# Performance work log

Measured on AMD Instinct MI355X. Metric: run time of the kernel, lower is better.

The kernel has to match this reference:

```python
import jax, jax.numpy as jnp
import numpy as np


def setup_inputs() -> dict:
    key = jax.random.key(0)
    k1, k2 = jax.random.split(key)
    x = jax.random.normal(k1, (1, 48, 56, 56), dtype=jnp.float32)
    w = jax.random.normal(k2, (24, 96, 7), dtype=jnp.float32)
    return {"x": x, "w": w, "shift": 1}


def reference(x, w, shift):
    # The torch unfold + einsum is a grouped cross-correlation along W:
    #   x viewed as (1, groups=2, Cin=24, H=56, W=56)
    #   out[l,o,k,n,m] = sum_{i,j} x[l,o,i,n, m+j-3] * w[i,k,j]   (zero-padded)
    # Same weight w is shared by both groups -> duplicate it per group.
    wt = jnp.transpose(w, (1, 0, 2))               # (96, 24, 7)  OIK per group
    kernel = jnp.concatenate([wt, wt], axis=0)     # (192, 24, 7) both groups
    kernel = kernel[:, :, None, :]                 # (O=192, I=24, KH=1, KW=7)
    y = jax.lax.conv_general_dilated(
        x, kernel,
        window_strides=(1, 1),
        padding=((0, 0), (3, 3)),                  # 'same' along W only
        dimension_numbers=("NCHW", "OIHW", "NCHW"),
        feature_group_count=2,
    )                                              # (1, 192, 56, 56)
    # torch.roll(t, shift, dims=2): roll along H
    return jnp.roll(y, shift, axis=2)
```

## Files before the change

### kernel.cpp

```cpp
#include <hip/hip_runtime.h>


#define Hh 56
#define Wd 56
#define HWsz (Hh * Wd)
#define CI 24
#define KW 7
#define OCB 4

__global__ __launch_bounds__(128) void conv7_roll_kernel(
    const float* __restrict__ x,
    const float* __restrict__ w,
    const int* __restrict__ shift_p,
    float* __restrict__ out)
{
    const int tid  = threadIdx.x;
    const int wid  = tid >> 6;
    const int lane = tid & 63;
    const int rl   = lane >> 4;
    const int c4r  = lane & 15;
    const int c4   = c4r < 13 ? c4r : 13;

    const int obase = blockIdx.x * OCB;
    const int g     = obase / 96;
    const int ocb96 = obase - g * 96;

    __shared__ __align__(16) float wl[OCB * CI * 8];
    for (int t = tid; t < OCB * CI * 8; t += 128) {
        const int oc_l = t / (CI * 8);
        const int rem  = t - oc_l * (CI * 8);
        const int ci   = rem >> 3;
        const int k    = rem & 7;
        wl[t] = (k < KW) ? w[ci * (96 * KW) + (ocb96 + oc_l) * KW + k] : 0.0f;
    }
    __syncthreads();

    const int shift = shift_p[0];
    const int h_out = blockIdx.y * 4 + rl;
    int hi = (h_out - shift) % Hh;
    if (hi < 0) hi += Hh;

    const float* xp = x + g * (CI * HWsz) + hi * Wd + c4 * 4;
    const float* lp = xp + (c4 > 0  ? -4 : 0);
    const float* rp = xp + (c4 < 13 ?  4 : 0);
    const bool lz = (c4 == 0);
    const bool rz = (c4 >= 13);

    const float* wl0 = &wl[(wid * 2    ) * (CI * 8)];
    const float* wl1 = &wl[(wid * 2 + 1) * (CI * 8)];

    float a0[4] = {0.f, 0.f, 0.f, 0.f};
    float a1[4] = {0.f, 0.f, 0.f, 0.f};

    #pragma unroll 4
    for (int ci = 0; ci < CI; ++ci) {
        float4 M = *(const float4*)(xp + ci * HWsz);
        float4 L = *(const float4*)(lp + ci * HWsz);
        float4 R = *(const float4*)(rp + ci * HWsz);
        if (lz) { L.x = 0.f; L.y = 0.f; L.z = 0.f; L.w = 0.f; }
        if (rz) { R.x = 0.f; R.y = 0.f; R.z = 0.f; R.w = 0.f; }
        float xv[12] = {L.x, L.y, L.z, L.w, M.x, M.y, M.z, M.w, R.x, R.y, R.z, R.w};

        float4 wa = *(const float4*)(wl0 + ci * 8);
        float4 wb = *(const float4*)(wl0 + ci * 8 + 4);
        float4 wc = *(const float4*)(wl1 + ci * 8);
        float4 wd = *(const float4*)(wl1 + ci * 8 + 4);
        float w0[7] = {wa.x, wa.y, wa.z, wa.w, wb.x, wb.y, wb.z};
        float w1[7] = {wc.x, wc.y, wc.z, wc.w, wd.x, wd.y, wd.z};

        #pragma unroll
        for (int k = 0; k < KW; ++k) {
            #pragma unroll
            for (int j = 0; j < 4; ++j) {
                a0[j] += xv[1 + j + k] * w0[k];
                a1[j] += xv[1 + j + k] * w1[k];
            }
        }
    }

    if (c4r < 14) {
        const int o0 = obase + wid * 2;
        float* op0 = out + o0 * HWsz + h_out * Wd + c4 * 4;
        float* op1 = op0 + HWsz;
        *(float4*)op0 = make_float4(a0[0], a0[1], a0[2], a0[3]);
        *(float4*)op1 = make_float4(a1[0], a1[1], a1[2], a1[3]);
    }
}

extern "C" void kernel_launch(void* const* d_in, const int* in_sizes, int n_in,
                              void* d_out, int out_size, void* d_ws, size_t ws_size,
                              hipStream_t stream)
{
    const float* x     = (const float*)d_in[0];
    const float* w     = (const float*)d_in[1];
    const int*   shift = (const int*)d_in[2];
    float*       out   = (float*)d_out;

    dim3 grid(48, 14);
    conv7_roll_kernel<<<grid, 128, 0, stream>>>(x, w, shift, out);
}
```

Baseline: 68.66 us.

## Share neighbor pixels via DPP lane shifts and prefetch input channels into registers

The left and right neighbor float4 global loads are replaced with DPP row_shr/row_shl lane shifts of the centre vector. Each 16-lane row covers one image row, and bound_ctrl zeroes the edge lanes to act as padding. This cuts input loads per channel from three to one. A 12-deep register ring buffer of input channels is also issued before the weight staging and barrier, so global latency overlaps the shared-memory fill. The cost is more register pressure from a fully unrolled loop holding 12 float4 prefetches.

```diff
diff --git a/kernel.cpp b/kernel.cpp
--- a/kernel.cpp
+++ b/kernel.cpp
@@ -7,6 +7,16 @@
 #define CI 24
 #define KW 7
 #define OCB 4
+#define PF 12
+
+__device__ __forceinline__ float dpp_shr1(float v) {
+    return __int_as_float(__builtin_amdgcn_update_dpp(
+        0, __float_as_int(v), 0x111, 0xF, 0xF, true));
+}
+__device__ __forceinline__ float dpp_shl1(float v) {
+    return __int_as_float(__builtin_amdgcn_update_dpp(
+        0, __float_as_int(v), 0x101, 0xF, 0xF, true));
+}
 
 __global__ __launch_bounds__(128) void conv7_roll_kernel(
     const float* __restrict__ x,
@@ -21,9 +31,23 @@
     const int c4r  = lane & 15;
     const int c4   = c4r < 13 ? c4r : 13;
 
+    const int shift = shift_p[0];
+
     const int obase = blockIdx.x * OCB;
     const int g     = obase / 96;
     const int ocb96 = obase - g * 96;
+
+    const int h_out = blockIdx.y * 4 + rl;
+    int hi = (h_out - shift) % Hh;
+    if (hi < 0) hi += Hh;
+
+    const float* xg = x + g * (CI * HWsz) + hi * Wd + c4 * 4;
+    const bool rz = (c4 >= 13);
+
+    float4 Mb[PF];
+    #pragma unroll
+    for (int p = 0; p < PF; ++p)
+        Mb[p] = *(const float4*)(xg + p * HWsz);
 
     __shared__ __align__(16) float wl[OCB * CI * 8];
     for (int t = tid; t < OCB * CI * 8; t += 128) {
@@ -35,30 +59,26 @@
     }
     __syncthreads();
 
-    const int shift = shift_p[0];
-    const int h_out = blockIdx.y * 4 + rl;
-    int hi = (h_out - shift) % Hh;
-    if (hi < 0) hi += Hh;
-
-    const float* xp = x + g * (CI * HWsz) + hi * Wd + c4 * 4;
-    const float* lp = xp + (c4 > 0  ? -4 : 0);
-    const float* rp = xp + (c4 < 13 ?  4 : 0);
-    const bool lz = (c4 == 0);
-    const bool rz = (c4 >= 13);
-
     const float* wl0 = &wl[(wid * 2    ) * (CI * 8)];
     const float* wl1 = &wl[(wid * 2 + 1) * (CI * 8)];
 
     float a0[4] = {0.f, 0.f, 0.f, 0.f};
     float a1[4] = {0.f, 0.f, 0.f, 0.f};
 
-    #pragma unroll 4
+    #pragma unroll
     for (int ci = 0; ci < CI; ++ci) {
-        float4 M = *(const float4*)(xp + ci * HWsz);
-        float4 L = *(const float4*)(lp + ci * HWsz);
-        float4 R = *(const float4*)(rp + ci * HWsz);
-        if (lz) { L.x = 0.f; L.y = 0.f; L.z = 0.f; L.w = 0.f; }
+        const int s = ci % PF;
+        float4 M = Mb[s];
+        if (ci + PF < CI)
+            Mb[s] = *(const float4*)(xg + (ci + PF) * HWsz);
+
+        float4 L, R;
+        L.x = dpp_shr1(M.x); L.y = dpp_shr1(M.y);
+        L.z = dpp_shr1(M.z); L.w = dpp_shr1(M.w);
+        R.x = dpp_shl1(M.x); R.y = dpp_shl1(M.y);
+        R.z = dpp_shl1(M.z); R.w = dpp_shl1(M.w);
         if (rz) { R.x = 0.f; R.y = 0.f; R.z = 0.f; R.w = 0.f; }
+
         float xv[12] = {L.x, L.y, L.z, L.w, M.x, M.y, M.z, M.w, R.x, R.y, R.z, R.w};
 
         float4 wa = *(const float4*)(wl0 + ci * 8);
```

Result: slower. 73.17 us (+6.6%).
